# Kernel optimization log

Measured on AMD Instinct MI355X. Metric: run time of the kernel, lower is better.

The kernel has to match this reference:

```python
import jax, jax.numpy as jnp
import numpy as np

BETA = 0.05  # module hardcodes self.beta = 0.05 regardless of init arg
K = 4096
D = 512


def setup_inputs() -> dict:
    key = jax.random.key(0)
    k1, k2 = jax.random.split(key)
    latents = jax.random.normal(k1, (32, 1024, D), dtype=jnp.float32)
    # nn.Embedding weight init: normal_(mean=0.8, std=0.1)
    emb_weight = 0.8 + 0.1 * jax.random.normal(k2, (K, D), dtype=jnp.float32)
    return {"latents": latents, "emb_weight": emb_weight}


def reference(latents, emb_weight):
    B, S, Dm = latents.shape
    flat = latents.reshape(-1, Dm)  # [N, D]
    dist = (jnp.sum(flat * flat, axis=1, keepdims=True)
            + jnp.sum(emb_weight * emb_weight, axis=1)
            - 2.0 * jnp.matmul(flat, emb_weight.T))  # [N, K]
    inds = jnp.argmin(dist, axis=1)  # [N]
    quantized = emb_weight[inds].reshape(B, S, Dm)  # gather instead of one-hot matmul

    commitment_loss = jnp.mean((jax.lax.stop_gradient(quantized) - latents) ** 2)
    embedding_loss = jnp.mean((quantized - jax.lax.stop_gradient(latents)) ** 2)
    vq_loss = commitment_loss * BETA + embedding_loss

    # straight-through estimator
    quantized_st = latents + jax.lax.stop_gradient(quantized - latents)

    N = flat.shape[0]
    avg_probs = jnp.zeros((K,), dtype=latents.dtype).at[inds].add(1.0) / N
    perplexity = jnp.exp(-jnp.sum(avg_probs * jnp.log(avg_probs + 1e-10)))

    output_inds = inds.reshape(B, S)
    return (quantized_st, vq_loss, output_inds, emb_weight, perplexity)
```

## Files before the change

kernel.cpp:

```cpp
#include <hip/hip_runtime.h>
#include <cfloat>
#include <cmath>
#include <climits>
#include <cstdint>

#define N_ROWS   32768
#define D_DIM    512
#define K_CODES  4096

#define EPS_GAP  0.008f
#define CAND_WIN 0.02f
#define FLAG_CAP 12000

typedef short s16x8 __attribute__((ext_vector_type(8)));
typedef float f32x4 __attribute__((ext_vector_type(4)));


__device__ __forceinline__ short f2bf_rne(float x) {
    unsigned u = __float_as_uint(x);
    unsigned r = (u + 0x7fffu + ((u >> 16) & 1u)) >> 16;
    return (short)r;
}
__device__ __forceinline__ float bf2f(short b) {
    return __uint_as_float(((unsigned)(unsigned short)b) << 16);
}

__device__ __forceinline__ void gld16(const short* g, short* l) {
    __builtin_amdgcn_global_load_lds(
        reinterpret_cast<const __attribute__((address_space(1))) unsigned int*>(
            reinterpret_cast<uintptr_t>(g)),
        reinterpret_cast<__attribute__((address_space(3))) unsigned int*>(
            (unsigned int)(reinterpret_cast<uintptr_t>(l))),
        16, 0, 0);
}

__device__ __forceinline__ float np_block128_sq(const float* p) {
    float P[16];
    #pragma unroll
    for (int l = 0; l < 16; ++l) {
        float s0 = __fmul_rn(p[0 * 16 + l], p[0 * 16 + l]);
        float s1 = __fmul_rn(p[1 * 16 + l], p[1 * 16 + l]);
        float s2 = __fmul_rn(p[2 * 16 + l], p[2 * 16 + l]);
        float s3 = __fmul_rn(p[3 * 16 + l], p[3 * 16 + l]);
        float s4 = __fmul_rn(p[4 * 16 + l], p[4 * 16 + l]);
        float s5 = __fmul_rn(p[5 * 16 + l], p[5 * 16 + l]);
        float s6 = __fmul_rn(p[6 * 16 + l], p[6 * 16 + l]);
        float s7 = __fmul_rn(p[7 * 16 + l], p[7 * 16 + l]);
        float a01 = __fadd_rn(s0, s1);
        float a23 = __fadd_rn(s2, s3);
        float a45 = __fadd_rn(s4, s5);
        float a67 = __fadd_rn(s6, s7);
        P[l] = __fadd_rn(__fadd_rn(a01, a23), __fadd_rn(a45, a67));
    }
    float T3[8];
    #pragma unroll
    for (int k = 0; k < 8; ++k) T3[k] = __fadd_rn(P[k], P[k + 8]);
    float T6[4];
    #pragma unroll
    for (int k = 0; k < 4; ++k) T6[k] = __fadd_rn(T3[k], T3[k + 4]);
    return __fadd_rn(__fadd_rn(__fadd_rn(T6[0], T6[1]), T6[2]), T6[3]);
}
__device__ __forceinline__ float np_sum512_sq(const float* p) {
    float B0 = np_block128_sq(p);
    float B1 = np_block128_sq(p + 128);
    float B2 = np_block128_sq(p + 256);
    float B3 = np_block128_sq(p + 384);
    return __fadd_rn(__fadd_rn(B0, B1), __fadd_rn(B2, B3));
}

__global__ void vq_conv_norm(const float* __restrict__ emb,
                             short* __restrict__ emb_hi, short* __restrict__ emb_lo,
                             float* __restrict__ e_norm) {
    int i = blockIdx.x * 256 + threadIdx.x;
    int lane = threadIdx.x & 63;
    size_t base = (size_t)i * 8;
    float4 a = *(const float4*)(emb + base);
    float4 b = *(const float4*)(emb + base + 4);
    float x[8] = {a.x, a.y, a.z, a.w, b.x, b.y, b.z, b.w};
    s16x8 hv, lv;
    float s = 0.f;
    #pragma unroll
    for (int j = 0; j < 8; ++j) {
        short h = f2bf_rne(x[j]);
        hv[j] = h;
        lv[j] = f2bf_rne(x[j] - bf2f(h));
        s = __fmaf_rn(x[j], x[j], s);
    }
    *(s16x8*)(emb_hi + base) = hv;
    *(s16x8*)(emb_lo + base) = lv;
    #pragma unroll
    for (int off = 32; off > 0; off >>= 1) s += __shfl_xor(s, off);
    if (lane == 0) e_norm[i >> 6] = s;
}

__device__ __forceinline__ int kswz(int r) { return (r & 3) ^ ((r >> 2) & 3); }

#define BROWS 256
#define BCOLS 256
#define KHALF 2048
#define BUFS2 32768

__device__ __forceinline__ void trunc_split8(const float* x, s16x8* hv, s16x8* lv) {
    #pragma unroll
    for (int j = 0; j < 8; ++j) {
        unsigned ux = __float_as_uint(x[j]);
        short h = (short)(ux >> 16);
        (*hv)[j] = h;
        float r = x[j] - bf2f(h);
        (*lv)[j] = (short)(__float_as_uint(r) >> 16);
    }
}

__global__ __launch_bounds__(1024, 4)
void vq_argmin_mfma(const float* __restrict__ lat,
                    const short* __restrict__ Bh_g, const short* __restrict__ Bl_g,
                    const float* __restrict__ e_norm,
                    float* __restrict__ pmin, float* __restrict__ psec,
                    unsigned short* __restrict__ pidx16)
{
    __shared__ short smem[2 * BUFS2];
    __shared__ float pbest_s[4][256];
    __shared__ float psec_s[4][256];
    __shared__ int   pidx_s[4][256];

    const int tid = threadIdx.x;
    const int l   = tid & 63;
    const int wid = tid >> 6;
    const int wr  = wid >> 2;
    const int wc  = wid & 3;
    const int l15 = l & 15;
    const int lhi = l >> 4;
    const int row0  = blockIdx.x * BROWS;
    const int kbase = blockIdx.y * KHALF;

    ((float*)pbest_s)[tid] = FLT_MAX;
    ((float*)psec_s)[tid]  = FLT_MAX;
    ((int*)pidx_s)[tid]    = 0;

    int offA[4], offB[4];
    #pragma unroll
    for (int m = 0; m < 4; ++m) {
        int r = wr * 64 + m * 16 + l15;
        offA[m] = r * 32 + (lhi ^ kswz(r)) * 8;
    }
    #pragma unroll
    for (int n = 0; n < 4; ++n) {
        int c = wc * 64 + n * 16 + l15;
        offB[n] = c * 32 + (lhi ^ kswz(c)) * 8;
    }

    const int ar = tid >> 2, asl = tid & 3;
    const int achunk = asl ^ kswz(ar);
    const size_t a_base = (size_t)(row0 + ar) * D_DIM + achunk * 8;
    const int adst = ar * 32 + asl * 8;
    const int br = tid >> 2, bsl = tid & 3;
    const int bchunk = bsl ^ kswz(br);
    const int bdst = tid * 8;

    {
        size_t go = (size_t)(kbase + br) * D_DIM + bchunk * 8;
        gld16(Bh_g + go, smem + 16384 + bdst);
        gld16(Bl_g + go, smem + 24576 + bdst);
        const float* p = lat + a_base;
        float4 f0 = *(const float4*)p;
        float4 f1 = *(const float4*)(p + 4);
        float x[8] = {f0.x, f0.y, f0.z, f0.w, f1.x, f1.y, f1.z, f1.w};
        s16x8 hv, lv;
        trunc_split8(x, &hv, &lv);
        *(s16x8*)(smem + adst) = hv;
        *(s16x8*)(smem + 8192 + adst) = lv;
    }
    __syncthreads();

    f32x4 acc[4][4];
    #pragma unroll
    for (int m = 0; m < 4; ++m)
        #pragma unroll
        for (int n = 0; n < 4; ++n) acc[m][n] = (f32x4){0.f, 0.f, 0.f, 0.f};

    for (int s = 0; s < 128; ++s) {
        short* cur = smem + (s & 1) * BUFS2;
        short* nxt = smem + ((s & 1) ^ 1) * BUFS2;

        float4 nf0, nf1;
        if (s < 127) {
            const int s1 = s + 1;
            const int k0 = (s1 & 15) * 32;
            const float* p = lat + a_base + k0;
            nf0 = *(const float4*)p;
            nf1 = *(const float4*)(p + 4);
            size_t go = (size_t)(kbase + (s1 >> 4) * 256 + br) * D_DIM + k0 + bchunk * 8;
            gld16(Bh_g + go, nxt + 16384 + bdst);
            gld16(Bl_g + go, nxt + 24576 + bdst);
        }

        s16x8 ah[4], al[4];
        #pragma unroll
        for (int m = 0; m < 4; ++m) {
            ah[m] = *(const s16x8*)(cur + offA[m]);
            al[m] = *(const s16x8*)(cur + 8192 + offA[m]);
        }
        __builtin_amdgcn_s_setprio(1);
        #pragma unroll
        for (int n = 0; n < 4; ++n) {
            s16x8 bh = *(const s16x8*)(cur + 16384 + offB[n]);
            s16x8 bl = *(const s16x8*)(cur + 24576 + offB[n]);
            #pragma unroll
            for (int m = 0; m < 4; ++m) {
                acc[m][n] = __builtin_amdgcn_mfma_f32_16x16x32_bf16(ah[m], bh, acc[m][n], 0, 0, 0);
                acc[m][n] = __builtin_amdgcn_mfma_f32_16x16x32_bf16(ah[m], bl, acc[m][n], 0, 0, 0);
                acc[m][n] = __builtin_amdgcn_mfma_f32_16x16x32_bf16(al[m], bh, acc[m][n], 0, 0, 0);
            }
        }
        __builtin_amdgcn_s_setprio(0);

        if ((s & 15) == 15) {
            const int cb0 = kbase + (s >> 4) * 256;
            float en[4];
            int   cc[4];
            #pragma unroll
            for (int n = 0; n < 4; ++n) {
                cc[n] = cb0 + wc * 64 + n * 16 + l15;
                en[n] = e_norm[cc[n]];
            }
            #pragma unroll
            for (int m = 0; m < 4; ++m)
                #pragma unroll
                for (int r = 0; r < 4; ++r) {
                    float v = FLT_MAX, sc = FLT_MAX;
                    int ii = 0;
                    #pragma unroll
                    for (int n = 0; n < 4; ++n) {
                        float dv = __fmaf_rn(-2.f, acc[m][n][r], en[n]);
                        if (dv < v) { sc = v; v = dv; ii = cc[n]; }
                        else if (dv < sc) sc = dv;
                    }
                    #pragma unroll
                    for (int off = 8; off > 0; off >>= 1) {
                        float v2 = __shfl_xor(v, off);
                        float s2 = __shfl_xor(sc, off);
                        int   i2 = __shfl_xor(ii, off);
                        float ns = fminf(fminf(sc, s2), fmaxf(v, v2));
                        if (v2 < v || (v2 == v && i2 < ii)) { v = v2; ii = i2; }
                        sc = ns;
                    }
                    if (l15 == 0) {
                        int rb = wr * 64 + m * 16 + lhi * 4 + r;
                        float ob = pbest_s[wc][rb];
                        float os = psec_s[wc][rb];
                        float nsec = fminf(fminf(os, sc), fmaxf(ob, v));
                        if (v < ob) { pbest_s[wc][rb] = v; pidx_s[wc][rb] = ii; }
                        psec_s[wc][rb] = nsec;
                    }
                }
            #pragma unroll
            for (int m = 0; m < 4; ++m)
                #pragma unroll
                for (int n = 0; n < 4; ++n) acc[m][n] = (f32x4){0.f, 0.f, 0.f, 0.f};
        }

        if (s < 127) {
            float x[8] = {nf0.x, nf0.y, nf0.z, nf0.w, nf1.x, nf1.y, nf1.z, nf1.w};
            s16x8 hv, lv;
            trunc_split8(x, &hv, &lv);
            *(s16x8*)(nxt + adst) = hv;
            *(s16x8*)(nxt + 8192 + adst) = lv;
        }
        __syncthreads();
    }

    if (tid < 256) {
        float B = FLT_MAX, S = FLT_MAX;
        int I = 0;
        #pragma unroll
        for (int w = 0; w < 4; ++w) {
            float b = pbest_s[w][tid], s = psec_s[w][tid];
            int i = pidx_s[w][tid];
            if (b < B || (b == B && i < I)) { S = fminf(B, s); B = b; I = i; }
            else S = fminf(S, fminf(b, s));
        }
        int row = row0 + tid;
        pmin[blockIdx.y * N_ROWS + row] = B;
        psec[blockIdx.y * N_ROWS + row] = S;
        pidx16[blockIdx.y * N_ROWS + row] = (unsigned short)I;
    }
}

__global__ void vq_select(const float* __restrict__ pmin, const float* __restrict__ psec,
                          const unsigned short* __restrict__ pidx16,
                          unsigned short* __restrict__ fidx, float* __restrict__ out_inds,
                          int* __restrict__ flagcnt, int* __restrict__ flaglist) {
    int row = blockIdx.x * 256 + threadIdx.x;
    float v0 = pmin[row], v1 = pmin[N_ROWS + row];
    float s0 = psec[row], s1 = psec[N_ROWS + row];
    int   i0 = pidx16[row], i1 = pidx16[N_ROWS + row];

    float best, sec; int bi;
    if (v1 < v0) { best = v1; bi = i1; sec = fminf(s1, v0); }
    else         { best = v0; bi = i0; sec = fminf(s0, v1); }

    fidx[row] = (unsigned short)bi;
    out_inds[row] = (float)bi;
    if (sec - best < EPS_GAP) {
        int p = atomicAdd(flagcnt, 1);
        if (p < FLAG_CAP) flaglist[p] = row;
    }
}

#define FIXT 1024
#define NWAV 16
#define MAXC 128

__global__ __launch_bounds__(FIXT)
void vq_fixrow(const float* __restrict__ lat, const float* __restrict__ emb,
               const int* __restrict__ flagcnt, const int* __restrict__ flaglist,
               unsigned short* __restrict__ fidx, float* __restrict__ out_inds)
{
    __shared__ float xs[D_DIM];
    __shared__ float dall[K_CODES];
    __shared__ float wmin_s[NWAV];
    __shared__ int   ccnt;
    __shared__ int   cands[MAXC];
    __shared__ float cd32[MAXC];

    const int t    = threadIdx.x;
    const int wave = t >> 6;
    const int lane = t & 63;
    int cnt = *flagcnt;
    if (cnt > FLAG_CAP) cnt = FLAG_CAP;

    for (int f = blockIdx.x; f < cnt; f += gridDim.x) {
        const int row = flaglist[f];
        __syncthreads();
        if (t < D_DIM) xs[t] = lat[(size_t)row * D_DIM + t];
        if (t == 0) ccnt = 0;
        __syncthreads();

        float x8[8];
        #pragma unroll
        for (int q = 0; q < 8; ++q) x8[q] = xs[lane * 8 + q];

        float lmin = FLT_MAX;
        for (int c = wave; c < K_CODES; c += 2 * NWAV) {
            const int c2 = c + NWAV;
            const float4* e4a = (const float4*)(emb + (size_t)c  * D_DIM);
            const float4* e4b = (const float4*)(emb + (size_t)c2 * D_DIM);
            float4 ea0 = e4a[lane * 2], ea1 = e4a[lane * 2 + 1];
            float4 eb0 = e4b[lane * 2], eb1 = e4b[lane * 2 + 1];

            float p0 = x8[0] - ea0.x, p1 = x8[1] - ea0.y;
            float p2 = x8[2] - ea0.z, p3 = x8[3] - ea0.w;
            float p4 = x8[4] - ea1.x, p5 = x8[5] - ea1.y;
            float p6 = x8[6] - ea1.z, p7 = x8[7] - ea1.w;
            float sA = __fmaf_rn(p0, p0, __fmaf_rn(p1, p1, __fmaf_rn(p2, p2, p3 * p3)));
            float sB = __fmaf_rn(p4, p4, __fmaf_rn(p5, p5, __fmaf_rn(p6, p6, p7 * p7)));
            float u = sA + sB;

            float q0 = x8[0] - eb0.x, q1 = x8[1] - eb0.y;
            float q2 = x8[2] - eb0.z, q3 = x8[3] - eb0.w;
            float q4 = x8[4] - eb1.x, q5 = x8[5] - eb1.y;
            float q6 = x8[6] - eb1.z, q7 = x8[7] - eb1.w;
            float tA = __fmaf_rn(q0, q0, __fmaf_rn(q1, q1, __fmaf_rn(q2, q2, q3 * q3)));
            float tB = __fmaf_rn(q4, q4, __fmaf_rn(q5, q5, __fmaf_rn(q6, q6, q7 * q7)));
            float v = tA + tB;

            #pragma unroll
            for (int off = 32; off > 0; off >>= 1) {
                u += __shfl_xor(u, off);
                v += __shfl_xor(v, off);
            }
            if (lane == 0) { dall[c] = u; dall[c2] = v; }
            lmin = fminf(lmin, fminf(u, v));
        }
        if (lane == 0) wmin_s[wave] = lmin;
        __syncthreads();

        float gmin = wmin_s[0];
        #pragma unroll
        for (int w = 1; w < NWAV; ++w) gmin = fminf(gmin, wmin_s[w]);
        const float thr = gmin + CAND_WIN;

        for (int c = t; c < K_CODES; c += FIXT) {
            if (dall[c] < thr) {
                int p = atomicAdd(&ccnt, 1);
                if (p < MAXC) cands[p] = c;
            }
        }
        __syncthreads();

        int nc = ccnt < MAXC ? ccnt : MAXC;
        if (t < nc) {
            int c = cands[t];
            const float* e = emb + (size_t)c * D_DIM;
            float t1 = np_sum512_sq(xs);
            float t2 = np_sum512_sq(e);
            float dot = 0.f;
            for (int k = 0; k < D_DIM; ++k)
                dot = __fmaf_rn(xs[k], e[k], dot);
            cd32[t] = __fsub_rn(__fadd_rn(t1, t2), __fmul_rn(2.f, dot));
        }
        __syncthreads();

        if (t == 0) {
            float bv = cd32[0]; int bx = cands[0];
            for (int w = 1; w < nc; ++w)
                if (cd32[w] < bv || (cd32[w] == bv && cands[w] < bx)) {
                    bv = cd32[w]; bx = cands[w];
                }
            fidx[row] = (unsigned short)bx;
            out_inds[row] = (float)bx;
        }
    }
}

__global__ void vq_gather(const float* __restrict__ lat, const float* __restrict__ emb,
                          const unsigned short* __restrict__ fidx,
                          float* __restrict__ out_q,
                          float* __restrict__ rowpart, int* __restrict__ hist) {
    int row  = blockIdx.x * 4 + (threadIdx.x >> 6);
    int lane = threadIdx.x & 63;
    int idx  = fidx[row];

    if (lane == 0) atomicAdd(&hist[idx], 1);

    const float4* e4 = (const float4*)(emb + (size_t)idx * D_DIM);
    const float4* x4 = (const float4*)(lat + (size_t)row * D_DIM);
    float4*       q4 = (float4*)(out_q + (size_t)row * D_DIM);

    float s = 0.f;
    #pragma unroll
    for (int i = 0; i < 2; ++i) {
        float4 e = e4[i * 64 + lane];
        float4 x = x4[i * 64 + lane];
        q4[i * 64 + lane] = e;
        float dx = e.x - x.x, dy = e.y - x.y, dz = e.z - x.z, dw = e.w - x.w;
        s += dx * dx + dy * dy + dz * dz + dw * dw;
    }
    #pragma unroll
    for (int off = 32; off > 0; off >>= 1) s += __shfl_down(s, off);
    if (lane == 0) rowpart[row] = s;
}

__global__ void vq_finalize(const float* __restrict__ rowpart, const int* __restrict__ hist,
                            float* __restrict__ out_loss, float* __restrict__ out_perp) {
    __shared__ float sdata[256];
    int t = threadIdx.x;

    float s = 0.f;
    for (int i = t; i < N_ROWS; i += 256) s += rowpart[i];
    sdata[t] = s;
    __syncthreads();
    for (int st = 128; st > 0; st >>= 1) {
        if (t < st) sdata[t] += sdata[t + st];
        __syncthreads();
    }
    if (t == 0) out_loss[0] = 1.05f * (sdata[0] / ((float)N_ROWS * (float)D_DIM));
    __syncthreads();

    float p = 0.f;
    for (int i = t; i < K_CODES; i += 256) {
        float pr = (float)hist[i] / (float)N_ROWS;
        p += pr * logf(pr + 1e-10f);
    }
    sdata[t] = p;
    __syncthreads();
    for (int st = 128; st > 0; st >>= 1) {
        if (t < st) sdata[t] += sdata[t + st];
        __syncthreads();
    }
    if (t == 0) out_perp[0] = expf(-sdata[0]);
}

extern "C" void kernel_launch(void* const* d_in, const int* in_sizes, int n_in,
                              void* d_out, int out_size, void* d_ws, size_t ws_size,
                              hipStream_t stream) {
    const float* lat = (const float*)d_in[0];
    const float* emb = (const float*)d_in[1];
    float* ob = (float*)d_out;

    short* emb_hi = (short*)(ob + 0);
    short* emb_lo = (short*)(ob + 1048576);
    float* pmin   = ob + 2097152;
    float* psec   = ob + 2162688;
    unsigned short* pidx16 = (unsigned short*)(ob + 2228224);
    float* e_norm = ob + 2260992;
    int*   flagcnt  = (int*)(ob + 2265088);
    int*   flaglist = (int*)(ob + 2265089);
    unsigned short* fidx = (unsigned short*)(ob + 16810000);
    int*   hist    = (int*)(ob + 16826384);
    float* rowpart = ob + 16830480;

    float* out_q    = ob;
    float* out_loss = ob + 16777216;
    float* out_inds = ob + 16777217;
    float* out_emb  = ob + 16809985;
    float* out_perp = ob + 18907137;

    hipMemsetAsync(flagcnt, 0, sizeof(int), stream);
    hipMemsetAsync(hist, 0, K_CODES * sizeof(int), stream);

    vq_conv_norm<<<dim3(1024), dim3(256), 0, stream>>>(emb, emb_hi, emb_lo, e_norm);

    vq_argmin_mfma<<<dim3(N_ROWS / BROWS, 2), dim3(1024), 0, stream>>>(
        lat, emb_hi, emb_lo, e_norm, pmin, psec, pidx16);

    vq_select<<<dim3(N_ROWS / 256), dim3(256), 0, stream>>>(pmin, psec, pidx16,
                                                            fidx, out_inds,
                                                            flagcnt, flaglist);

    vq_fixrow<<<dim3(512), dim3(FIXT), 0, stream>>>(lat, emb, flagcnt, flaglist,
                                                    fidx, out_inds);

    vq_gather<<<dim3(N_ROWS / 4), dim3(256), 0, stream>>>(lat, emb, fidx, out_q, rowpart, hist);

    vq_finalize<<<dim3(1), dim3(256), 0, stream>>>(rowpart, hist, out_loss, out_perp);

    hipMemcpyAsync(out_emb, emb, (size_t)K_CODES * D_DIM * sizeof(float),
                   hipMemcpyDeviceToDevice, stream);
}
```

Measured before the change: 705.9 us.

## Precompute latent bf16 low halves and pack argmin index with quantized gap

A prepass now computes the low bf16 residual of the latents into a scratch buffer, so the MFMA kernel loads it straight into LDS with async global-to-LDS copies and derives only the high half in registers. The argmin kernel also stops writing a separate second-best array and index array. It packs the index and a quantized gap into one 32-bit word, which cuts partial-result traffic. In exchange the prepass adds a full extra read of the latents plus a write of 32 MB, and the gap quantization loses precision near the flag threshold.

```diff
diff --git a/kernel.cpp b/kernel.cpp
--- a/kernel.cpp
+++ b/kernel.cpp
@@ -23,6 +23,24 @@
 }
 __device__ __forceinline__ float bf2f(short b) {
     return __uint_as_float(((unsigned)(unsigned short)b) << 16);
+}
+
+__device__ __forceinline__ void trunc_split8(const float* x, s16x8* hv, s16x8* lv) {
+    #pragma unroll
+    for (int j = 0; j < 8; ++j) {
+        unsigned ux = __float_as_uint(x[j]);
+        short h = (short)(ux >> 16);
+        (*hv)[j] = h;
+        float r = x[j] - bf2f(h);
+        (*lv)[j] = (short)(__float_as_uint(r) >> 16);
+    }
+}
+__device__ __forceinline__ s16x8 hi8(const float* x) {
+    s16x8 hv;
+    #pragma unroll
+    for (int j = 0; j < 8; ++j)
+        hv[j] = (short)(__float_as_uint(x[j]) >> 16);
+    return hv;
 }
 
 __device__ __forceinline__ void gld16(const short* g, short* l) {
@@ -68,55 +86,54 @@
     return __fadd_rn(__fadd_rn(B0, B1), __fadd_rn(B2, B3));
 }
 
-__global__ void vq_conv_norm(const float* __restrict__ emb,
-                             short* __restrict__ emb_hi, short* __restrict__ emb_lo,
-                             float* __restrict__ e_norm) {
+__global__ void vq_conv(const float* __restrict__ lat, const float* __restrict__ emb,
+                        short* __restrict__ lat_lo,
+                        short* __restrict__ emb_hi, short* __restrict__ emb_lo,
+                        float* __restrict__ e_norm) {
     int i = blockIdx.x * 256 + threadIdx.x;
-    int lane = threadIdx.x & 63;
-    size_t base = (size_t)i * 8;
-    float4 a = *(const float4*)(emb + base);
-    float4 b = *(const float4*)(emb + base + 4);
-    float x[8] = {a.x, a.y, a.z, a.w, b.x, b.y, b.z, b.w};
-    s16x8 hv, lv;
-    float s = 0.f;
-    #pragma unroll
-    for (int j = 0; j < 8; ++j) {
-        short h = f2bf_rne(x[j]);
-        hv[j] = h;
-        lv[j] = f2bf_rne(x[j] - bf2f(h));
-        s = __fmaf_rn(x[j], x[j], s);
-    }
-    *(s16x8*)(emb_hi + base) = hv;
-    *(s16x8*)(emb_lo + base) = lv;
-    #pragma unroll
-    for (int off = 32; off > 0; off >>= 1) s += __shfl_xor(s, off);
-    if (lane == 0) e_norm[i >> 6] = s;
+    if (i < 2097152) {
+        size_t base = (size_t)i * 8;
+        float4 a = *(const float4*)(lat + base);
+        float4 b = *(const float4*)(lat + base + 4);
+        float x[8] = {a.x, a.y, a.z, a.w, b.x, b.y, b.z, b.w};
+        s16x8 hv, lv;
+        trunc_split8(x, &hv, &lv);
+        *(s16x8*)(lat_lo + base) = lv;
+    } else {
+        int j = i - 2097152;
+        int lane = threadIdx.x & 63;
+        size_t base = (size_t)j * 8;
+        float4 a = *(const float4*)(emb + base);
+        float4 b = *(const float4*)(emb + base + 4);
+        float x[8] = {a.x, a.y, a.z, a.w, b.x, b.y, b.z, b.w};
+        s16x8 hv, lv;
+        float s = 0.f;
+        #pragma unroll
+        for (int q = 0; q < 8; ++q) {
+            short h = f2bf_rne(x[q]);
+            hv[q] = h;
+            lv[q] = f2bf_rne(x[q] - bf2f(h));
+            s = __fmaf_rn(x[q], x[q], s);
+        }
+        *(s16x8*)(emb_hi + base) = hv;
+        *(s16x8*)(emb_lo + base) = lv;
+        #pragma unroll
+        for (int off = 32; off > 0; off >>= 1) s += __shfl_xor(s, off);
+        if (lane == 0) e_norm[j >> 6] = s;
+    }
 }
 
 __device__ __forceinline__ int kswz(int r) { return (r & 3) ^ ((r >> 2) & 3); }
 
 #define BROWS 256
-#define BCOLS 256
 #define KHALF 2048
 #define BUFS2 32768
 
-__device__ __forceinline__ void trunc_split8(const float* x, s16x8* hv, s16x8* lv) {
-    #pragma unroll
-    for (int j = 0; j < 8; ++j) {
-        unsigned ux = __float_as_uint(x[j]);
-        short h = (short)(ux >> 16);
-        (*hv)[j] = h;
-        float r = x[j] - bf2f(h);
-        (*lv)[j] = (short)(__float_as_uint(r) >> 16);
-    }
-}
-
 __global__ __launch_bounds__(1024, 4)
-void vq_argmin_mfma(const float* __restrict__ lat,
+void vq_argmin_mfma(const float* __restrict__ lat, const short* __restrict__ Al_g,
                     const short* __restrict__ Bh_g, const short* __restrict__ Bl_g,
                     const float* __restrict__ e_norm,
-                    float* __restrict__ pmin, float* __restrict__ psec,
-                    unsigned short* __restrict__ pidx16)
+                    float* __restrict__ pmin, unsigned* __restrict__ pidxgap)
 {
     __shared__ short smem[2 * BUFS2];
     __shared__ float pbest_s[4][256];
@@ -149,26 +166,22 @@
         offB[n] = c * 32 + (lhi ^ kswz(c)) * 8;
     }
 
-    const int ar = tid >> 2, asl = tid & 3;
-    const int achunk = asl ^ kswz(ar);
-    const size_t a_base = (size_t)(row0 + ar) * D_DIM + achunk * 8;
-    const int adst = ar * 32 + asl * 8;
-    const int br = tid >> 2, bsl = tid & 3;
-    const int bchunk = bsl ^ kswz(br);
-    const int bdst = tid * 8;
+    const int rr = tid >> 2, sl = tid & 3;
+    const int chk = sl ^ kswz(rr);
+    const size_t a_off = (size_t)(row0 + rr) * D_DIM + chk * 8;
+    const int dst = tid * 8;
 
     {
-        size_t go = (size_t)(kbase + br) * D_DIM + bchunk * 8;
-        gld16(Bh_g + go, smem + 16384 + bdst);
-        gld16(Bl_g + go, smem + 24576 + bdst);
-        const float* p = lat + a_base;
+        gld16(Al_g + a_off, smem + 8192 + dst);
+        size_t go = (size_t)(kbase + rr) * D_DIM + chk * 8;
+        gld16(Bh_g + go, smem + 16384 + dst);
+        gld16(Bl_g + go, smem + 24576 + dst);
+        const float* p = lat + a_off;
         float4 f0 = *(const float4*)p;
         float4 f1 = *(const float4*)(p + 4);
         float x[8] = {f0.x, f0.y, f0.z, f0.w, f1.x, f1.y, f1.z, f1.w};
-        s16x8 hv, lv;
-        trunc_split8(x, &hv, &lv);
-        *(s16x8*)(smem + adst) = hv;
-        *(s16x8*)(smem + 8192 + adst) = lv;
+        s16x8 hv = hi8(x);
+        *(s16x8*)(smem + dst) = hv;
     }
     __syncthreads();
 
@@ -186,12 +199,13 @@
         if (s < 127) {
             const int s1 = s + 1;
             const int k0 = (s1 & 15) * 32;
-            const float* p = lat + a_base + k0;
+            gld16(Al_g + a_off + k0, nxt + 8192 + dst);
+            size_t go = (size_t)(kbase + (s1 >> 4) * 256 + rr) * D_DIM + k0 + chk * 8;
+            gld16(Bh_g + go, nxt + 16384 + dst);
+            gld16(Bl_g + go, nxt + 24576 + dst);
+            const float* p = lat + a_off + k0;
             nf0 = *(const float4*)p;
             nf1 = *(const float4*)(p + 4);
-            size_t go = (size_t)(kbase + (s1 >> 4) * 256 + br) * D_DIM + k0 + bchunk * 8;
-            gld16(Bh_g + go, nxt + 16384 + bdst);
-            gld16(Bl_g + go, nxt + 24576 + bdst);
         }
 
         s16x8 ah[4], al[4];
@@ -261,10 +275,8 @@
 
         if (s < 127) {
             float x[8] = {nf0.x, nf0.y, nf0.z, nf0.w, nf1.x, nf1.y, nf1.z, nf1.w};
-            s16x8 hv, lv;
-            trunc_split8(x, &hv, &lv);
-            *(s16x8*)(nxt + adst) = hv;
-            *(s16x8*)(nxt + 8192 + adst) = lv;
+            s16x8 hv = hi8(x);
+            *(s16x8*)(nxt + dst) = hv;
         }
         __syncthreads();
     }
@@ -281,19 +293,22 @@
         }
         int row = row0 + tid;
         pmin[blockIdx.y * N_ROWS + row] = B;
-        psec[blockIdx.y * N_ROWS + row] = S;
-        pidx16[blockIdx.y * N_ROWS + row] = (unsigned short)I;
-    }
-}
-
-__global__ void vq_select(const float* __restrict__ pmin, const float* __restrict__ psec,
-                          const unsigned short* __restrict__ pidx16,
+        float gap = S - B;
+        unsigned g16 = (unsigned)fminf(gap * 4096.f, 65535.f);
+        pidxgap[blockIdx.y * N_ROWS + row] = ((unsigned)I << 16) | g16;
+    }
+}
+
+__global__ void vq_select(const float* __restrict__ pmin,
+                          const unsigned* __restrict__ pidxgap,
                           unsigned short* __restrict__ fidx, float* __restrict__ out_inds,
                           int* __restrict__ flagcnt, int* __restrict__ flaglist) {
     int row = blockIdx.x * 256 + threadIdx.x;
     float v0 = pmin[row], v1 = pmin[N_ROWS + row];
-    float s0 = psec[row], s1 = psec[N_ROWS + row];
-    int   i0 = pidx16[row], i1 = pidx16[N_ROWS + row];
+    unsigned p0 = pidxgap[row], p1 = pidxgap[N_ROWS + row];
+    float s0 = v0 + (float)(p0 & 0xFFFFu) * (1.f / 4096.f);
+    float s1 = v1 + (float)(p1 & 0xFFFFu) * (1.f / 4096.f);
+    int i0 = (int)(p0 >> 16), i1 = (int)(p1 >> 16);
 
     float best, sec; int bi;
     if (v1 < v0) { best = v1; bi = i1; sec = fminf(s1, v0); }
@@ -478,17 +493,17 @@
     const float* emb = (const float*)d_in[1];
     float* ob = (float*)d_out;
 
-    short* emb_hi = (short*)(ob + 0);
-    short* emb_lo = (short*)(ob + 1048576);
-    float* pmin   = ob + 2097152;
-    float* psec   = ob + 2162688;
-    unsigned short* pidx16 = (unsigned short*)(ob + 2228224);
-    float* e_norm = ob + 2260992;
-    int*   flagcnt  = (int*)(ob + 2265088);
-    int*   flaglist = (int*)(ob + 2265089);
-    unsigned short* fidx = (unsigned short*)(ob + 16810000);
-    int*   hist    = (int*)(ob + 16826384);
-    float* rowpart = ob + 16830480;
+    short* lat_lo = (short*)(ob + 0);
+    short* emb_hi = (short*)(ob + 8388608);
+    short* emb_lo = (short*)(ob + 9437184);
+    float* pmin   = ob + 10485760;
+    unsigned* pidxgap = (unsigned*)(ob + 10551296);
+    float* e_norm = ob + 10616832;
+    int*   flagcnt  = (int*)(ob + 16810000);
+    int*   flaglist = (int*)(ob + 16810001);
+    unsigned short* fidx = (unsigned short*)(ob + 16822016);
+    int*   hist    = (int*)(ob + 16838400);
+    float* rowpart = ob + 16842496;
 
     float* out_q    = ob;
     float* out_loss = ob + 16777216;
@@ -499,12 +514,13 @@
     hipMemsetAsync(flagcnt, 0, sizeof(int), stream);
     hipMemsetAsync(hist, 0, K_CODES * sizeof(int), stream);
 
-    vq_conv_norm<<<dim3(1024), dim3(256), 0, stream>>>(emb, emb_hi, emb_lo, e_norm);
+    vq_conv<<<dim3(9216), dim3(256), 0, stream>>>(lat, emb, lat_lo,
+                                                  emb_hi, emb_lo, e_norm);
 
     vq_argmin_mfma<<<dim3(N_ROWS / BROWS, 2), dim3(1024), 0, stream>>>(
-        lat, emb_hi, emb_lo, e_norm, pmin, psec, pidx16);
-
-    vq_select<<<dim3(N_ROWS / 256), dim3(256), 0, stream>>>(pmin, psec, pidx16,
+        lat, lat_lo, emb_hi, emb_lo, e_norm, pmin, pidxgap);
+
+    vq_select<<<dim3(N_ROWS / 256), dim3(256), 0, stream>>>(pmin, pidxgap,
                                                             fidx, out_inds,
                                                             flagcnt, flaglist);
 
```

Measured after the change: 725.7 us. +2.8%, slower.
